# Performance work log

Measured on AMD Instinct MI355X. Metric: run time of the kernel, lower is better.

## Reference

```python
import jax, jax.numpy as jnp
import numpy as np

N = 50000        # nodes
E = 1600000      # edges (before self loops)
IN_DIM = 300     # input feature size
HID = 256        # hidden size
HEADS = 8
OC = HID // HEADS  # out channels per head = 32
LAYERS = 4
B = 1024         # number of target pairs
C = 3            # num classes
NEG_SLOPE = 0.2  # PyG GATConv leaky_relu slope


def setup_inputs() -> dict:
    key = jax.random.key(0)
    ks = jax.random.split(key, 12)

    def glorot(k, shape):
        lim = np.sqrt(6.0 / (shape[-2] + shape[-1]))
        return jax.random.uniform(k, shape, jnp.float32, -lim, lim)

    return {
        "x": jax.random.normal(ks[0], (N, IN_DIM), jnp.float32),
        "edge_index": jax.random.randint(ks[1], (2, E), 0, N, jnp.int64 if jax.config.jax_enable_x64 else jnp.int32),
        "target_mask": jax.random.randint(ks[2], (B, 2), 0, N, jnp.int64 if jax.config.jax_enable_x64 else jnp.int32),
        # lin1: [IN_DIM, HID] (stored pre-transposed vs torch)
        "lin1_W": glorot(ks[3], (IN_DIM, HID)),
        "lin1_b": jnp.zeros((HID,), jnp.float32),
        # stacked GATConv params
        "convs_W": glorot(ks[4], (LAYERS, HID, HEADS * OC)),
        "convs_att_dst": glorot(ks[5], (LAYERS, HEADS, OC)),  # att half applied to x_i (target)
        "convs_att_src": glorot(ks[6], (LAYERS, HEADS, OC)),  # att half applied to x_j (source)
        "convs_b": jnp.zeros((LAYERS, HID), jnp.float32),
        # lin3: [2*HID, C]
        "lin3_W": glorot(ks[7], (2 * HID, C)),
        "lin3_b": jnp.zeros((C,), jnp.float32),
    }


def gat_layer(h, src, tgt, W, att_dst, att_src, bias):
    """PyG-style GATConv (concat heads), edge list already includes self loops.
    h: [N, HID]; src/tgt: [E+N]; W: [HID, HEADS*OC]."""
    hw = (h @ W).reshape(N, HEADS, OC)
    # per-node attention scores, gathered per-edge (avoids materializing concat features)
    s_dst = jnp.einsum("nho,ho->nh", hw, att_dst)  # score for target role
    s_src = jnp.einsum("nho,ho->nh", hw, att_src)  # score for source role
    alpha = jax.nn.leaky_relu(s_dst[tgt] + s_src[src], NEG_SLOPE)  # [Etot, HEADS]
    # softmax over edges sharing the same target node (self loops => no empty segments)
    m = jax.ops.segment_max(alpha, tgt, num_segments=N)
    ex = jnp.exp(alpha - m[tgt])
    denom = jax.ops.segment_sum(ex, tgt, num_segments=N)
    a = ex / (denom[tgt] + 1e-16)
    # weighted scatter-aggregate of source features
    out = jax.ops.segment_sum(hw[src] * a[:, :, None], tgt, num_segments=N)  # [N, HEADS, OC]
    return out.reshape(N, HEADS * OC) + bias


def reference(x, edge_index, target_mask, lin1_W, lin1_b, convs_W,
              convs_att_dst, convs_att_src, convs_b, lin3_W, lin3_b):
    # add self loops once (PyG GATConv does this per layer; same edge set every layer)
    loop = jnp.arange(N, dtype=edge_index.dtype)
    src = jnp.concatenate([edge_index[0], loop])
    tgt = jnp.concatenate([edge_index[1], loop])

    h = x @ lin1_W + lin1_b
    for l in range(LAYERS):
        h = jax.nn.elu(gat_layer(h, src, tgt, convs_W[l],
                                 convs_att_dst[l], convs_att_src[l], convs_b[l]))
    # gather the two target nodes per sample and flatten -> [B, 2*HID]
    feats = h[target_mask].reshape(B, 2 * HID)
    logits = feats @ lin3_W + lin3_b
    return logits
```

## Files before the change

### kernel.cpp

```cpp
#include <hip/hip_runtime.h>
#include <math.h>

#define N_NODES 50000
#define N_PAD   50048
#define E_EDGES 1600000
#define ETOT    (E_EDGES + N_NODES)
#define EPAD    (E_EDGES + 8 * N_NODES)
#define IN_DIM  300
#define KP1     320
#define HID     256
#define HEADS   8
#define OC      32
#define LAYERS  4
#define BSAMP   1024
#define NEG_SLOPE 0.2f
#define DEG_CAP 128

#define NB     8
#define NPB    6250
#define BCAP   262144
#define NBLK_P 512
#define NBLK_S 196

typedef unsigned long long ull;
typedef _Float16 half8 __attribute__((ext_vector_type(8)));
typedef _Float16 half4v __attribute__((ext_vector_type(4)));
typedef float f32x4 __attribute__((ext_vector_type(4)));

#define GLDS16(g, l) __builtin_amdgcn_global_load_lds( \
    (const __attribute__((address_space(1))) void*)(g), \
    (__attribute__((address_space(3))) void*)(l), 16, 0, 0)


__global__ __launch_bounds__(256) void part_count_kernel(const int* __restrict__ tgt,
                                                         int* __restrict__ gcount) {
    __shared__ int cnt[NB];
    if (threadIdx.x < NB) cnt[threadIdx.x] = 0;
    __syncthreads();
    const int chunk = (ETOT + NBLK_P - 1) / NBLK_P;
    int beg = blockIdx.x * chunk;
    int end = min(beg + chunk, ETOT);
    for (int e = beg + threadIdx.x; e < end; e += 256) {
        int t_ = (e < E_EDGES) ? tgt[e] : (e - E_EDGES);
        atomicAdd(&cnt[t_ / NPB], 1);
    }
    __syncthreads();
    if (threadIdx.x < NB) gcount[blockIdx.x * NB + threadIdx.x] = cnt[threadIdx.x];
}

__global__ __launch_bounds__(64) void part_scan_kernel(const int* __restrict__ gcount,
                                                       int* __restrict__ goff,
                                                       int* __restrict__ bcnt) {
    int b = threadIdx.x;
    if (b >= NB) return;
    int running = 0;
    for (int k = 0; k < NBLK_P; k++) {
        goff[k * NB + b] = running;
        running += gcount[k * NB + b];
    }
    bcnt[b] = running;
}

__global__ __launch_bounds__(256) void part_scatter_kernel(const int* __restrict__ src,
                                                           const int* __restrict__ tgt,
                                                           const int* __restrict__ goff,
                                                           ull* __restrict__ bpart) {
    __shared__ int cur[NB];
    if (threadIdx.x < NB) cur[threadIdx.x] = goff[blockIdx.x * NB + threadIdx.x];
    __syncthreads();
    const int chunk = (ETOT + NBLK_P - 1) / NBLK_P;
    int beg = blockIdx.x * chunk;
    int end = min(beg + chunk, ETOT);
    for (int e = beg + threadIdx.x; e < end; e += 256) {
        int s_, t_;
        if (e < E_EDGES) { s_ = src[e]; t_ = tgt[e]; }
        else             { s_ = t_ = e - E_EDGES; }
        int b = t_ / NPB;
        int pos = atomicAdd(&cur[b], 1);
        bpart[(size_t)b * BCAP + pos] = ((ull)(unsigned)t_ << 32) | (unsigned)s_;
    }
}

__global__ __launch_bounds__(256) void count_edges_kernel(const ull* __restrict__ bpart,
                                                          const int* __restrict__ bcnt,
                                                          int* counts) {
    int b = blockIdx.x & (NB - 1);
    int ib = blockIdx.x >> 3;
    int nblk = gridDim.x >> 3;
    int nb = bcnt[b];
    const ull* bp = bpart + (size_t)b * BCAP;
    for (int i = ib * 256 + threadIdx.x; i < nb; i += nblk * 256)
        atomicAdd(&counts[(int)(bp[i] >> 32)], 1);
}

__global__ __launch_bounds__(256) void scan1_kernel(const int* __restrict__ counts,
                                                    int* __restrict__ row_ptr,
                                                    int* __restrict__ bsum) {
    __shared__ int sums[256];
    int t = threadIdx.x;
    int i = blockIdx.x * 256 + t;
    int c = (i < N_NODES) ? ((counts[i] + 7) & ~7) : 0;
    sums[t] = c;
    __syncthreads();
    for (int off = 1; off < 256; off <<= 1) {
        int a = sums[t];
        int u = (t >= off) ? sums[t - off] : 0;
        __syncthreads();
        sums[t] = a + u;
        __syncthreads();
    }
    if (i < N_NODES) row_ptr[i] = sums[t] - c;
    if (t == 255) bsum[blockIdx.x] = sums[255];
}

__global__ __launch_bounds__(256) void scan2_kernel(const int* __restrict__ bsum,
                                                    int* __restrict__ boff,
                                                    int* __restrict__ row_ptr) {
    __shared__ int sums[256];
    int t = threadIdx.x;
    int b = (t < NBLK_S) ? bsum[t] : 0;
    sums[t] = b;
    __syncthreads();
    for (int off = 1; off < 256; off <<= 1) {
        int a = sums[t];
        int u = (t >= off) ? sums[t - off] : 0;
        __syncthreads();
        sums[t] = a + u;
        __syncthreads();
    }
    if (t < NBLK_S) boff[t] = sums[t] - b;
    if (t == 255) row_ptr[N_NODES] = sums[255];
}

__global__ __launch_bounds__(256) void scan3_kernel(int* __restrict__ row_ptr,
                                                    const int* __restrict__ boff,
                                                    int* __restrict__ cursor) {
    int i = blockIdx.x * 256 + threadIdx.x;
    if (i >= N_NODES) return;
    int v = row_ptr[i] + boff[blockIdx.x];
    row_ptr[i] = v;
    cursor[i]  = v;
}

__global__ __launch_bounds__(256) void fill_edges_kernel(const ull* __restrict__ bpart,
                                                         const int* __restrict__ bcnt,
                                                         int* cursor, int* __restrict__ col) {
    int b = blockIdx.x & (NB - 1);
    int ib = blockIdx.x >> 3;
    int nblk = gridDim.x >> 3;
    int nb = bcnt[b];
    const ull* bp = bpart + (size_t)b * BCAP;
    for (int i = ib * 256 + threadIdx.x; i < nb; i += nblk * 256) {
        ull pk = bp[i];
        int t_ = (int)(pk >> 32);
        int s_ = (int)pk;
        int pos = atomicAdd(&cursor[t_], 1);
        col[pos] = s_;
    }
}

__global__ __launch_bounds__(256) void pad_edges_kernel(const int* __restrict__ cursor,
                                                        const int* __restrict__ row_ptr,
                                                        int* __restrict__ col) {
    int i = blockIdx.x * 256 + threadIdx.x;
    if (i >= N_NODES) return;
    int e = cursor[i];
    int pe = row_ptr[i + 1];
    for (; e < pe; e++) col[e] = i;
}


__global__ __launch_bounds__(256) void cast_x_kernel(const float* __restrict__ x, _Float16* __restrict__ xh) {
    long i = (long)blockIdx.x * 256 + threadIdx.x;
    if (i >= (long)N_NODES * KP1) return;
    int r = (int)(i / KP1), c = (int)(i % KP1);
    float v = (c < IN_DIM) ? x[(size_t)r * IN_DIM + c] : 0.f;
    xh[i] = (_Float16)v;
}

__global__ __launch_bounds__(256) void cast_w1_kernel(const float* __restrict__ W, _Float16* __restrict__ Wt) {
    int i = blockIdx.x * 256 + threadIdx.x;
    if (i >= HID * KP1) return;
    int n = i / KP1, k = i % KP1;
    float v = (k < IN_DIM) ? W[(size_t)k * HID + n] : 0.f;
    Wt[i] = (_Float16)v;
}

__global__ __launch_bounds__(256) void cast_wc_kernel(const float* __restrict__ W, _Float16* __restrict__ Wt) {
    int i = blockIdx.x * 256 + threadIdx.x;
    if (i >= LAYERS * HID * HID) return;
    int l = i / (HID * HID);
    int r = i % (HID * HID);
    int n = r / HID, k = r % HID;
    Wt[i] = (_Float16)W[(size_t)l * HID * HID + (size_t)k * HID + n];
}

__global__ __launch_bounds__(256) void gemm_mfma_kernel(const _Float16* __restrict__ A,
                                                        const _Float16* __restrict__ Wt,
                                                        const float* __restrict__ bias,
                                                        _Float16* __restrict__ C,
                                                        int M, int Kp, int addbias) {
    __shared__ _Float16 As[128][32];
    __shared__ _Float16 Bs[128][32];
    const int tid = threadIdx.x;
    const int m0 = blockIdx.x * 128;
    const int n0 = blockIdx.y * 128;
    const int w = tid >> 6, lane = tid & 63;
    const int wm = (w & 1) * 64, wn = (w >> 1) * 64;
    const int quad = lane >> 4, m16 = lane & 15;

    f32x4 acc[4][4];
    #pragma unroll
    for (int i = 0; i < 4; i++)
        #pragma unroll
        for (int j = 0; j < 4; j++)
            acc[i][j] = (f32x4){0.f, 0.f, 0.f, 0.f};

    char* lA = (char*)&As[0][0] + w * 1024;
    char* lB = (char*)&Bs[0][0] + w * 1024;

    for (int k0 = 0; k0 < Kp; k0 += 32) {
        #pragma unroll
        for (int i = 0; i < 2; i++) {
            int seg = tid + i * 256;
            int row = seg >> 2, off = seg & 3;
            GLDS16(&A[(size_t)(m0 + row) * Kp + k0 + off * 8], lA + i * 4096);
            GLDS16(&Wt[(size_t)(n0 + row) * Kp + k0 + off * 8], lB + i * 4096);
        }
        __syncthreads();

        half8 af[4], bf[4];
        #pragma unroll
        for (int i = 0; i < 4; i++) {
            af[i] = *(const half8*)&As[wm + i * 16 + m16][quad * 8];
            bf[i] = *(const half8*)&Bs[wn + i * 16 + m16][quad * 8];
        }
        #pragma unroll
        for (int mi = 0; mi < 4; mi++)
            #pragma unroll
            for (int ni = 0; ni < 4; ni++)
                acc[mi][ni] = __builtin_amdgcn_mfma_f32_16x16x32_f16(af[mi], bf[ni], acc[mi][ni], 0, 0, 0);
        __syncthreads();
    }

    #pragma unroll
    for (int mi = 0; mi < 4; mi++) {
        #pragma unroll
        for (int r = 0; r < 4; r++) {
            int row = m0 + wm + mi * 16 + quad * 4 + r;
            if (row < M) {
                #pragma unroll
                for (int ni = 0; ni < 4; ni++) {
                    int colg = n0 + wn + ni * 16 + m16;
                    float v = acc[mi][ni][r];
                    if (addbias) v += bias[colg];
                    C[(size_t)row * HID + colg] = (_Float16)v;
                }
            }
        }
    }
}

__global__ __launch_bounds__(256) void score_kernel(const _Float16* __restrict__ hw,
                                                    const float* __restrict__ att_dst,
                                                    const float* __restrict__ att_src,
                                                    float* __restrict__ s_dst,
                                                    float* __restrict__ s_src) {
    int wv = threadIdx.x >> 6, lane = threadIdx.x & 63;
    int nd = lane >> 3, hd = lane & 7;
    float4 ad[8], as4[8];
    const float4* A4d = (const float4*)att_dst;
    const float4* A4s = (const float4*)att_src;
    #pragma unroll
    for (int j = 0; j < 8; j++) { ad[j] = A4d[hd * 8 + j]; as4[j] = A4s[hd * 8 + j]; }
    const half8* hw8 = (const half8*)hw;
    int nwaves = gridDim.x * 4;
    for (int g = blockIdx.x * 4 + wv; g < N_NODES / 8; g += nwaves) {
        int node = g * 8 + nd;
        float sd = 0.f, ss = 0.f;
        #pragma unroll
        for (int k = 0; k < 4; k++) {
            half8 v = hw8[(size_t)node * 32 + hd * 4 + k];
            #pragma unroll
            for (int i = 0; i < 8; i++) {
                float f = (float)v[i];
                int q = k * 8 + i;
                sd += f * ((const float*)&ad[q >> 2])[q & 3];
                ss += f * ((const float*)&as4[q >> 2])[q & 3];
            }
        }
        s_dst[(size_t)g * 64 + lane] = sd;
        s_src[(size_t)g * 64 + lane] = ss;
    }
}

__global__ __launch_bounds__(256) void agg_kernel(const int* __restrict__ row_ptr,
                                                  const int* __restrict__ deg_arr,
                                                  const int* __restrict__ col,
                                                  const float* __restrict__ s_dst,
                                                  const float* __restrict__ s_src,
                                                  const _Float16* __restrict__ hw,
                                                  const float* __restrict__ bias,
                                                  _Float16* __restrict__ h_out) {
    __shared__ float exL[4][DEG_CAP * 8];
    __shared__ int  snL[4][DEG_CAP];

    int wv   = threadIdx.x >> 6;
    int lane = threadIdx.x & 63;
    int t = blockIdx.x * 4 + wv;
    if (t >= N_NODES) return;

    int start = row_ptr[t];
    int pdeg  = row_ptr[t + 1] - start;
    int deg   = deg_arr[t];

    int eh  = lane & 7;
    int ech = lane >> 3;
    float sd = s_dst[(size_t)t * HEADS + eh];

    if (pdeg <= DEG_CAP) {
        int ngrp = pdeg >> 3;
        float dsum = 0.f;
        for (int g = 0; g < ngrp; g++) {
            int slot = g * 8 + ech;
            int sn = col[start + slot];
            float a = sd + s_src[(size_t)sn * HEADS + eh];
            a = (a > 0.f) ? a : NEG_SLOPE * a;
            float exv = (slot < deg) ? __expf(a) : 0.f;
            exL[wv][slot * 8 + eh] = exv;
            if (eh == 0) snL[wv][slot] = sn;
            dsum += exv;
        }
        dsum += __shfl_xor(dsum, 8);
        dsum += __shfl_xor(dsum, 16);
        dsum += __shfl_xor(dsum, 32);

        int p  = lane >> 5;
        int c  = lane & 31;
        int hh = c >> 2;
        float inv = 1.f / (__shfl(dsum, hh) + 1e-16f);

        const half8* hw8 = (const half8*)hw;
        float acc[8] = {0.f, 0.f, 0.f, 0.f, 0.f, 0.f, 0.f, 0.f};

        int g = 0;
        for (; g + 2 <= ngrp; g += 2) {
            int base = g * 8;
            int   sns[8];
            half8 v[8];
            float ex[8];
            #pragma unroll
            for (int j = 0; j < 8; j++) sns[j] = snL[wv][base + 2 * j + p];
            #pragma unroll
            for (int j = 0; j < 8; j++) v[j] = hw8[(size_t)sns[j] * 32 + c];
            #pragma unroll
            for (int j = 0; j < 8; j++) ex[j] = exL[wv][(base + 2 * j + p) * 8 + hh];
            #pragma unroll
            for (int j = 0; j < 8; j++)
                #pragma unroll
                for (int i = 0; i < 8; i++)
                    acc[i] += ex[j] * (float)v[j][i];
        }
        if (g < ngrp) {
            int base = g * 8;
            int   sns[4];
            half8 v[4];
            float ex[4];
            #pragma unroll
            for (int j = 0; j < 4; j++) sns[j] = snL[wv][base + 2 * j + p];
            #pragma unroll
            for (int j = 0; j < 4; j++) v[j] = hw8[(size_t)sns[j] * 32 + c];
            #pragma unroll
            for (int j = 0; j < 4; j++) ex[j] = exL[wv][(base + 2 * j + p) * 8 + hh];
            #pragma unroll
            for (int j = 0; j < 4; j++)
                #pragma unroll
                for (int i = 0; i < 8; i++)
                    acc[i] += ex[j] * (float)v[j][i];
        }

        #pragma unroll
        for (int i = 0; i < 8; i++) acc[i] += __shfl_xor(acc[i], 32);

        if (p == 0) {
            half8 ov;
            #pragma unroll
            for (int i = 0; i < 8; i++) {
                float o = acc[i] * inv + bias[c * 8 + i];
                o = (o > 0.f) ? o : (__expf(o) - 1.f);
                ov[i] = (_Float16)o;
            }
            ((half8*)h_out)[(size_t)t * 32 + c] = ov;
        }
    } else {
        int end = start + deg;
        float mx = -1e30f;
        for (int base = start; base < end; base += 8) {
            int e = base + ech;
            if (e < end) {
                int sn = col[e];
                float a = sd + s_src[(size_t)sn * HEADS + eh];
                a = (a > 0.f) ? a : NEG_SLOPE * a;
                mx = fmaxf(mx, a);
            }
        }
        mx = fmaxf(mx, __shfl_xor(mx, 8));
        mx = fmaxf(mx, __shfl_xor(mx, 16));
        mx = fmaxf(mx, __shfl_xor(mx, 32));

        float4 acc = {0.f, 0.f, 0.f, 0.f};
        float dsum = 0.f;
        const half4v* hw4 = (const half4v*)hw;
        int chead = lane >> 3;
        for (int base = start; base < end; base += 8) {
            int e = base + ech;
            float exv = 0.f;
            int sn = 0;
            if (e < end) {
                sn = col[e];
                float a = sd + s_src[(size_t)sn * HEADS + eh];
                a = (a > 0.f) ? a : NEG_SLOPE * a;
                exv = __expf(a - mx);
                dsum += exv;
            }
            int cnt = min(8, end - base);
            for (int j = 0; j < cnt; j++) {
                float exj = __shfl(exv, j * 8 + chead);
                int  snj  = __shfl(sn,  j * 8);
                half4v v = hw4[(size_t)snj * 64 + lane];
                acc.x += exj * (float)v[0];
                acc.y += exj * (float)v[1];
                acc.z += exj * (float)v[2];
                acc.w += exj * (float)v[3];
            }
        }
        dsum += __shfl_xor(dsum, 8);
        dsum += __shfl_xor(dsum, 16);
        dsum += __shfl_xor(dsum, 32);
        float den = __shfl(dsum, chead) + 1e-16f;
        float inv = 1.f / den;
        int cb = lane * 4;
        float o[4] = {acc.x * inv + bias[cb + 0], acc.y * inv + bias[cb + 1],
                      acc.z * inv + bias[cb + 2], acc.w * inv + bias[cb + 3]};
        #pragma unroll
        for (int i = 0; i < 4; i++) o[i] = (o[i] > 0.f) ? o[i] : (__expf(o[i]) - 1.f);
        half4v ov;
        ov[0] = (_Float16)o[0]; ov[1] = (_Float16)o[1];
        ov[2] = (_Float16)o[2]; ov[3] = (_Float16)o[3];
        ((half4v*)h_out)[(size_t)t * 64 + lane] = ov;
    }
}

__global__ __launch_bounds__(256) void head_kernel(const _Float16* __restrict__ h,
                                                   const int* __restrict__ target_mask,
                                                   const float* __restrict__ W,
                                                   const float* __restrict__ b,
                                                   float* __restrict__ out) {
    int s = blockIdx.x;
    int t = threadIdx.x;
    int n0 = target_mask[s * 2 + 0];
    int n1 = target_mask[s * 2 + 1];
    float f0 = (float)h[(size_t)n0 * HID + t];
    float f1 = (float)h[(size_t)n1 * HID + t];
    float a0 = f0 * W[t * 3 + 0] + f1 * W[(t + 256) * 3 + 0];
    float a1 = f0 * W[t * 3 + 1] + f1 * W[(t + 256) * 3 + 1];
    float a2 = f0 * W[t * 3 + 2] + f1 * W[(t + 256) * 3 + 2];
    #pragma unroll
    for (int off = 32; off >= 1; off >>= 1) {
        a0 += __shfl_xor(a0, off);
        a1 += __shfl_xor(a1, off);
        a2 += __shfl_xor(a2, off);
    }
    __shared__ float red[4][3];
    int wv = t >> 6, ln = t & 63;
    if (ln == 0) { red[wv][0] = a0; red[wv][1] = a1; red[wv][2] = a2; }
    __syncthreads();
    if (t < 3) {
        out[s * 3 + t] = red[0][t] + red[1][t] + red[2][t] + red[3][t] + b[t];
    }
}


extern "C" void kernel_launch(void* const* d_in, const int* in_sizes, int n_in,
                              void* d_out, int out_size, void* d_ws, size_t ws_size,
                              hipStream_t stream) {
    const float* x        = (const float*)d_in[0];
    const int*   eidx     = (const int*)  d_in[1];
    const int*   tmask    = (const int*)  d_in[2];
    const float* lin1_W   = (const float*)d_in[3];
    const float* lin1_b   = (const float*)d_in[4];
    const float* convs_W  = (const float*)d_in[5];
    const float* att_dst  = (const float*)d_in[6];
    const float* att_src  = (const float*)d_in[7];
    const float* convs_b  = (const float*)d_in[8];
    const float* lin3_W   = (const float*)d_in[9];
    const float* lin3_b   = (const float*)d_in[10];
    float* out = (float*)d_out;

    char* ws = (char*)d_ws;
    size_t off = 0;
    auto alloc = [&](size_t bytes) -> void* {
        void* p = ws + off;
        off = (off + bytes + 255) & ~(size_t)255;
        return p;
    };
    _Float16* xh   = (_Float16*)alloc((size_t)N_PAD * KP1 * 2);
    _Float16* h    = (_Float16*)alloc((size_t)N_PAD * HID * 2);
    _Float16* hw   = (_Float16*)alloc((size_t)N_NODES * HID * 2);
    _Float16* w1t  = (_Float16*)alloc((size_t)HID * KP1 * 2);
    _Float16* wct  = (_Float16*)alloc((size_t)LAYERS * HID * HID * 2);
    float* sdst    = (float*)alloc((size_t)N_NODES * HEADS * 4);
    float* ssrc    = (float*)alloc((size_t)N_NODES * HEADS * 4);
    int*   counts  = (int*)  alloc((size_t)N_NODES * 4);
    int*   rowptr  = (int*)  alloc((size_t)(N_NODES + 1) * 4);
    int*   cursor  = (int*)  alloc((size_t)N_NODES * 4);
    int*   col     = (int*)  alloc((size_t)EPAD * 4);
    ull*   bpart   = (ull*)  alloc((size_t)NB * BCAP * 8);
    int*   bcnt    = (int*)  alloc((size_t)NB * 4);
    int*   gcount  = (int*)  alloc((size_t)NBLK_P * NB * 4);
    int*   goff    = (int*)  alloc((size_t)NBLK_P * NB * 4);
    int*   bsum    = (int*)  alloc((size_t)NBLK_S * 4);
    int*   boff    = (int*)  alloc((size_t)NBLK_S * 4);

    const int* src = eidx;
    const int* tgt = eidx + E_EDGES;

    hipMemsetAsync(counts, 0, (size_t)N_NODES * 4, stream);
    part_count_kernel<<<NBLK_P, 256, 0, stream>>>(tgt, gcount);
    part_scan_kernel<<<1, 64, 0, stream>>>(gcount, goff, bcnt);
    part_scatter_kernel<<<NBLK_P, 256, 0, stream>>>(src, tgt, goff, bpart);
    count_edges_kernel<<<256, 256, 0, stream>>>(bpart, bcnt, counts);
    scan1_kernel<<<NBLK_S, 256, 0, stream>>>(counts, rowptr, bsum);
    scan2_kernel<<<1, 256, 0, stream>>>(bsum, boff, rowptr);
    scan3_kernel<<<NBLK_S, 256, 0, stream>>>(rowptr, boff, cursor);
    fill_edges_kernel<<<256, 256, 0, stream>>>(bpart, bcnt, cursor, col);
    pad_edges_kernel<<<(N_NODES + 255) / 256, 256, 0, stream>>>(cursor, rowptr, col);

    cast_x_kernel<<<((long)N_NODES * KP1 + 255) / 256, 256, 0, stream>>>(x, xh);
    cast_w1_kernel<<<(HID * KP1 + 255) / 256, 256, 0, stream>>>(lin1_W, w1t);
    cast_wc_kernel<<<(LAYERS * HID * HID + 255) / 256, 256, 0, stream>>>(convs_W, wct);

    gemm_mfma_kernel<<<dim3((N_NODES + 127) / 128, HID / 128), 256, 0, stream>>>(
        xh, w1t, lin1_b, h, N_NODES, KP1, 1);

    for (int l = 0; l < LAYERS; l++) {
        gemm_mfma_kernel<<<dim3((N_NODES + 127) / 128, HID / 128), 256, 0, stream>>>(
            h, wct + (size_t)l * HID * HID, nullptr, hw, N_NODES, HID, 0);
        score_kernel<<<256, 256, 0, stream>>>(
            hw, att_dst + (size_t)l * HEADS * OC, att_src + (size_t)l * HEADS * OC, sdst, ssrc);
        agg_kernel<<<(N_NODES + 3) / 4, 256, 0, stream>>>(
            rowptr, counts, col, sdst, ssrc, hw, convs_b + (size_t)l * HID, h);
    }

    head_kernel<<<BSAMP, 256, 0, stream>>>(h, tmask, lin3_W, lin3_b, out);
}
```

Baseline: 975.7 us.

## Parallelize partition scan, vectorize x cast, simplify aggregation loop

The serial 8-thread partition offset scan becomes a 512-thread Hillis-Steele scan in shared memory, removing a long single-thread-per-bucket dependency chain. The x-to-fp16 cast now writes 8 halves per thread using float4 loads instead of one element per thread. The aggregation kernel drops its 8-edge unrolled main loop and uses only the 4-edge loop body, which reduces register pressure but leaves fewer gather loads in flight per iteration.

```diff
diff --git a/kernel.cpp b/kernel.cpp
--- a/kernel.cpp
+++ b/kernel.cpp
@@ -48,17 +48,35 @@
     if (threadIdx.x < NB) gcount[blockIdx.x * NB + threadIdx.x] = cnt[threadIdx.x];
 }
 
-__global__ __launch_bounds__(64) void part_scan_kernel(const int* __restrict__ gcount,
-                                                       int* __restrict__ goff,
-                                                       int* __restrict__ bcnt) {
-    int b = threadIdx.x;
-    if (b >= NB) return;
-    int running = 0;
-    for (int k = 0; k < NBLK_P; k++) {
-        goff[k * NB + b] = running;
-        running += gcount[k * NB + b];
-    }
-    bcnt[b] = running;
+__global__ __launch_bounds__(512) void part_scan_kernel(const int* __restrict__ gcount,
+                                                        int* __restrict__ goff,
+                                                        int* __restrict__ bcnt) {
+    __shared__ int arr[NBLK_P][NB];
+    int k = threadIdx.x;
+    int4 a = ((const int4*)gcount)[k * 2];
+    int4 b = ((const int4*)gcount)[k * 2 + 1];
+    int own[NB] = {a.x, a.y, a.z, a.w, b.x, b.y, b.z, b.w};
+    #pragma unroll
+    for (int j = 0; j < NB; j++) arr[k][j] = own[j];
+    __syncthreads();
+    for (int off = 1; off < NBLK_P; off <<= 1) {
+        int tmp[NB];
+        #pragma unroll
+        for (int j = 0; j < NB; j++) tmp[j] = (k >= off) ? arr[k - off][j] : 0;
+        __syncthreads();
+        #pragma unroll
+        for (int j = 0; j < NB; j++) arr[k][j] += tmp[j];
+        __syncthreads();
+    }
+    int ex[NB];
+    #pragma unroll
+    for (int j = 0; j < NB; j++) ex[j] = arr[k][j] - own[j];
+    ((int4*)goff)[k * 2]     = make_int4(ex[0], ex[1], ex[2], ex[3]);
+    ((int4*)goff)[k * 2 + 1] = make_int4(ex[4], ex[5], ex[6], ex[7]);
+    if (k == NBLK_P - 1) {
+        #pragma unroll
+        for (int j = 0; j < NB; j++) bcnt[j] = arr[k][j];
+    }
 }
 
 __global__ __launch_bounds__(256) void part_scatter_kernel(const int* __restrict__ src,
@@ -171,11 +189,24 @@
 
 
 __global__ __launch_bounds__(256) void cast_x_kernel(const float* __restrict__ x, _Float16* __restrict__ xh) {
-    long i = (long)blockIdx.x * 256 + threadIdx.x;
-    if (i >= (long)N_NODES * KP1) return;
-    int r = (int)(i / KP1), c = (int)(i % KP1);
-    float v = (c < IN_DIM) ? x[(size_t)r * IN_DIM + c] : 0.f;
-    xh[i] = (_Float16)v;
+    int i = blockIdx.x * 256 + threadIdx.x;
+    if (i >= N_NODES * (KP1 / 8)) return;
+    int r = i / (KP1 / 8), c8 = i % (KP1 / 8);
+    half8 o;
+    const float4* xr = (const float4*)(x + (size_t)r * IN_DIM);
+    if (c8 < 37) {
+        float4 u = xr[c8 * 2], v = xr[c8 * 2 + 1];
+        o[0] = (_Float16)u.x; o[1] = (_Float16)u.y; o[2] = (_Float16)u.z; o[3] = (_Float16)u.w;
+        o[4] = (_Float16)v.x; o[5] = (_Float16)v.y; o[6] = (_Float16)v.z; o[7] = (_Float16)v.w;
+    } else if (c8 == 37) {
+        float4 u = xr[74];
+        o[0] = (_Float16)u.x; o[1] = (_Float16)u.y; o[2] = (_Float16)u.z; o[3] = (_Float16)u.w;
+        o[4] = o[5] = o[6] = o[7] = (_Float16)0.f;
+    } else {
+        #pragma unroll
+        for (int j = 0; j < 8; j++) o[j] = (_Float16)0.f;
+    }
+    ((half8*)xh)[i] = o;
 }
 
 __global__ __launch_bounds__(256) void cast_w1_kernel(const float* __restrict__ W, _Float16* __restrict__ Wt) {
@@ -343,25 +374,7 @@
         const half8* hw8 = (const half8*)hw;
         float acc[8] = {0.f, 0.f, 0.f, 0.f, 0.f, 0.f, 0.f, 0.f};
 
-        int g = 0;
-        for (; g + 2 <= ngrp; g += 2) {
-            int base = g * 8;
-            int   sns[8];
-            half8 v[8];
-            float ex[8];
-            #pragma unroll
-            for (int j = 0; j < 8; j++) sns[j] = snL[wv][base + 2 * j + p];
-            #pragma unroll
-            for (int j = 0; j < 8; j++) v[j] = hw8[(size_t)sns[j] * 32 + c];
-            #pragma unroll
-            for (int j = 0; j < 8; j++) ex[j] = exL[wv][(base + 2 * j + p) * 8 + hh];
-            #pragma unroll
-            for (int j = 0; j < 8; j++)
-                #pragma unroll
-                for (int i = 0; i < 8; i++)
-                    acc[i] += ex[j] * (float)v[j][i];
-        }
-        if (g < ngrp) {
+        for (int g = 0; g < ngrp; g++) {
             int base = g * 8;
             int   sns[4];
             half8 v[4];
@@ -527,7 +540,7 @@
 
     hipMemsetAsync(counts, 0, (size_t)N_NODES * 4, stream);
     part_count_kernel<<<NBLK_P, 256, 0, stream>>>(tgt, gcount);
-    part_scan_kernel<<<1, 64, 0, stream>>>(gcount, goff, bcnt);
+    part_scan_kernel<<<1, NBLK_P, 0, stream>>>(gcount, goff, bcnt);
     part_scatter_kernel<<<NBLK_P, 256, 0, stream>>>(src, tgt, goff, bpart);
     count_edges_kernel<<<256, 256, 0, stream>>>(bpart, bcnt, counts);
     scan1_kernel<<<NBLK_S, 256, 0, stream>>>(counts, rowptr, bsum);
@@ -536,7 +549,7 @@
     fill_edges_kernel<<<256, 256, 0, stream>>>(bpart, bcnt, cursor, col);
     pad_edges_kernel<<<(N_NODES + 255) / 256, 256, 0, stream>>>(cursor, rowptr, col);
 
-    cast_x_kernel<<<((long)N_NODES * KP1 + 255) / 256, 256, 0, stream>>>(x, xh);
+    cast_x_kernel<<<(N_NODES * (KP1 / 8) + 255) / 256, 256, 0, stream>>>(x, xh);
     cast_w1_kernel<<<(HID * KP1 + 255) / 256, 256, 0, stream>>>(lin1_W, w1t);
     cast_wc_kernel<<<(LAYERS * HID * HID + 255) / 256, 256, 0, stream>>>(convs_W, wct);
 
```

After: 945.9 us. -3.1%, faster.
